# Kernel optimization log

Hardware: AMD Instinct MI355X
Metric: run time of the kernel (lower is better)

Reference implementation:

```python
import jax, jax.numpy as jnp
import numpy as np
import math

D_MODEL = 1024
NUM_HEADS = 16
SEQ = 2048
BATCH = 2


def setup_inputs() -> dict:
    key = jax.random.key(0)
    ks = jax.random.split(key, 12)
    s = 1.0 / math.sqrt(D_MODEL)
    inp = {
        "query": jax.random.normal(ks[0], (SEQ, BATCH, D_MODEL), jnp.float32),
        "key": jax.random.normal(ks[1], (SEQ, BATCH, D_MODEL), jnp.float32),
        "value": jax.random.normal(ks[2], (SEQ, BATCH, D_MODEL), jnp.float32),
        "Wq": jax.random.normal(ks[3], (D_MODEL, D_MODEL), jnp.float32) * s,
        "bq": jax.random.normal(ks[4], (D_MODEL,), jnp.float32) * 0.01,
        "Wk": jax.random.normal(ks[5], (D_MODEL, D_MODEL), jnp.float32) * s,
        "bk": jax.random.normal(ks[6], (D_MODEL,), jnp.float32) * 0.01,
        "Wv": jax.random.normal(ks[7], (D_MODEL, D_MODEL), jnp.float32) * s,
        "bv": jax.random.normal(ks[8], (D_MODEL,), jnp.float32) * 0.01,
        "Wo": jax.random.normal(ks[9], (D_MODEL, D_MODEL), jnp.float32) * s,
        "bo": jax.random.normal(ks[10], (D_MODEL,), jnp.float32) * 0.01,
    }
    # causal (subsequent) mask: True above the diagonal means masked
    inp["attn_mask"] = jnp.triu(jnp.ones((SEQ, SEQ), bool), k=1)
    # key_padding_mask: True = padding; random lengths in [SEQ//2, SEQ]
    lengths = jax.random.randint(ks[11], (BATCH,), SEQ // 2, SEQ + 1)
    inp["key_padding_mask"] = jnp.arange(SEQ)[None, :] >= lengths[:, None]
    return inp


def reference(query, key, value, Wq, bq, Wk, bk, Wv, bv, Wo, bo, attn_mask, key_padding_mask):
    S, B, D = query.shape
    H = NUM_HEADS
    dk = D // H

    def proj_split(x, W, b):
        y = x @ W.T + b                      # [S, B, D]
        return y.reshape(S, B, H, dk).transpose(1, 2, 0, 3)  # [B, H, S, dk]

    q = proj_split(query, Wq, bq)
    k = proj_split(key, Wk, bk)
    v = proj_split(value, Wv, bv)

    scores = jnp.einsum("bhqd,bhkd->bhqk", q, k) / jnp.sqrt(jnp.float32(dk))
    mask = key_padding_mask[:, None, None, :] | attn_mask[None, None, :, :]
    scores = jnp.where(mask, -jnp.inf, scores)
    p = jax.nn.softmax(scores, axis=-1)       # [B, H, S, S]
    x = jnp.einsum("bhqk,bhkd->bhqd", p, v)   # [B, H, S, dk]
    x = x.transpose(2, 0, 1, 3).reshape(S, B, D)
    return x @ Wo.T + bo
```

## Files before the change

kernel.cpp:

```cpp
#include <hip/hip_runtime.h>
#include <hip/hip_bf16.h>

#define S_LEN 2048
#define BATCH 2
#define DMODEL 1024
#define NHEAD 16
#define DK 64

typedef __bf16 bf16_t;
typedef bf16_t bf16x4 __attribute__((ext_vector_type(4)));
typedef bf16_t bf16x8 __attribute__((ext_vector_type(8)));
typedef float floatx4 __attribute__((ext_vector_type(4)));

#define SEG  ((size_t)S_LEN * BATCH * DMODEL)
#define WSEG ((size_t)DMODEL * DMODEL)
#define CVT_TOT (3 * SEG + 4 * WSEG)

#define QSCALE 0.180336879f

__global__ void prep_lens(const unsigned char* __restrict__ am,
                          const unsigned char* __restrict__ kpm,
                          int* __restrict__ lens)
{
    __shared__ int stride_s;
    __shared__ int cnt[BATCH];
    const int t = threadIdx.x;
    if (t == 0) {
        int st;
        if (am[1]) st = 1;
        else if (am[2] | am[3]) st = 2;
        else st = 4;
        stride_s = st;
    }
    if (t < BATCH) cnt[t] = 0;
    __syncthreads();
    const int st = stride_s;
    for (int idx = t; idx < BATCH * S_LEN; idx += blockDim.x) {
        int nz = 0;
        for (int c = 0; c < st; c++) nz |= kpm[idx * st + c];
        if (nz) atomicAdd(&cnt[idx / S_LEN], 1);
    }
    __syncthreads();
    if (t < BATCH) lens[t] = S_LEN - cnt[t];
}

__global__ void cvt_all(const float* __restrict__ q, const float* __restrict__ k,
                        const float* __restrict__ v, const float* __restrict__ wq,
                        const float* __restrict__ wk, const float* __restrict__ wv,
                        const float* __restrict__ wo, bf16_t* __restrict__ out)
{
    size_t i4 = ((size_t)blockIdx.x * blockDim.x + threadIdx.x) * 4;
    const size_t stride = (size_t)gridDim.x * blockDim.x * 4;
    for (; i4 < CVT_TOT; i4 += stride) {
        const float* src;
        size_t off;
        if (i4 < SEG)                    { src = q;  off = i4; }
        else if (i4 < 2 * SEG)           { src = k;  off = i4 - SEG; }
        else if (i4 < 3 * SEG)           { src = v;  off = i4 - 2 * SEG; }
        else if (i4 < 3 * SEG + WSEG)    { src = wq; off = i4 - 3 * SEG; }
        else if (i4 < 3 * SEG + 2 * WSEG){ src = wk; off = i4 - (3 * SEG + WSEG); }
        else if (i4 < 3 * SEG + 3 * WSEG){ src = wv; off = i4 - (3 * SEG + 2 * WSEG); }
        else                             { src = wo; off = i4 - (3 * SEG + 3 * WSEG); }
        const float4 x = *(const float4*)(src + off);
        bf16x4 r;
        r[0] = (bf16_t)x.x; r[1] = (bf16_t)x.y; r[2] = (bf16_t)x.z; r[3] = (bf16_t)x.w;
        *(bf16x4*)(out + i4) = r;
    }
}

__global__ __launch_bounds__(256, 2)
void gemm_qkv(const bf16_t* __restrict__ Abase, const bf16_t* __restrict__ Wbase,
              const float* __restrict__ bq, const float* __restrict__ bk,
              const float* __restrict__ bv, bf16_t* __restrict__ Obase)
{
    __shared__ bf16_t As[128 * 32];
    __shared__ bf16_t Bs[128 * 32];

    const int z = blockIdx.z;
    const bf16_t* A = Abase + (size_t)z * SEG;
    const bf16_t* W = Wbase + (size_t)z * WSEG;
    const float* bias = (z == 0) ? bq : (z == 1) ? bk : bv;
    bf16_t* C = Obase + (size_t)z * SEG;

    const int t    = threadIdx.x;
    const int wave = t >> 6;
    const int lane = t & 63;
    const int l15  = lane & 15;
    const int quad = lane >> 4;

    const int mBase = blockIdx.y * 128;
    const int nBase = blockIdx.x * 128;
    const int wRow  = (wave >> 1) * 64;
    const int wCol  = (wave & 1) * 64;

    floatx4 acc[4][4];
#pragma unroll
    for (int i = 0; i < 4; i++)
#pragma unroll
        for (int j = 0; j < 4; j++) acc[i][j] = (floatx4){0.f, 0.f, 0.f, 0.f};

    for (int k0 = 0; k0 < DMODEL; k0 += 32) {
#pragma unroll
        for (int c = 0; c < 2; c++) {
            const int chunk = c * 256 + t;
            const int row   = chunk >> 2;
            const int col   = (chunk & 3) * 8;
            const bf16_t* gA = A + (size_t)(mBase + row) * DMODEL + k0 + col;
            const bf16_t* gB = W + (size_t)(nBase + row) * DMODEL + k0 + col;
            bf16_t* lA = As + (c * 256 + wave * 64) * 8;
            bf16_t* lB = Bs + (c * 256 + wave * 64) * 8;
            __builtin_amdgcn_global_load_lds(
                (const __attribute__((address_space(1))) void*)gA,
                (__attribute__((address_space(3))) void*)lA, 16, 0, 0);
            __builtin_amdgcn_global_load_lds(
                (const __attribute__((address_space(1))) void*)gB,
                (__attribute__((address_space(3))) void*)lB, 16, 0, 0);
        }
        __syncthreads();

        bf16x8 af[4], bfr[4];
#pragma unroll
        for (int mi = 0; mi < 4; mi++)
            af[mi] = *(const bf16x8*)(As + (wRow + mi * 16 + l15) * 32 + quad * 8);
#pragma unroll
        for (int ni = 0; ni < 4; ni++)
            bfr[ni] = *(const bf16x8*)(Bs + (wCol + ni * 16 + l15) * 32 + quad * 8);
#pragma unroll
        for (int mi = 0; mi < 4; mi++)
#pragma unroll
            for (int ni = 0; ni < 4; ni++)
                acc[mi][ni] = __builtin_amdgcn_mfma_f32_16x16x32_bf16(
                    af[mi], bfr[ni], acc[mi][ni], 0, 0, 0);
        __syncthreads();
    }

    const float scale = (z == 0) ? QSCALE : 1.0f;
    float bvv[4];
#pragma unroll
    for (int ni = 0; ni < 4; ni++)
        bvv[ni] = bias[nBase + wCol + ni * 16 + l15];

#pragma unroll
    for (int mi = 0; mi < 4; mi++) {
#pragma unroll
        for (int ni = 0; ni < 4; ni++) {
            const int n = nBase + wCol + ni * 16 + l15;
            const int h = n >> 6, i = n & 63;
#pragma unroll
            for (int j = 0; j < 4; j++) {
                const int m = mBase + wRow + mi * 16 + quad * 4 + j;
                const int s = m >> 1, b = m & 1;
                const float v = (acc[mi][ni][j] + bvv[ni]) * scale;
                size_t off;
                if (z < 2)
                    off = ((size_t)(b * NHEAD + h) * S_LEN + s) * DK + i;
                else
                    off = ((size_t)(b * NHEAD + h) * DK + i) * S_LEN + s;
                C[off] = (bf16_t)v;
            }
        }
    }
}

__global__ __launch_bounds__(256, 3)
void attn(const bf16_t* __restrict__ qw, const bf16_t* __restrict__ kw,
          const bf16_t* __restrict__ vw, bf16_t* __restrict__ ow,
          const int* __restrict__ lens)
{
    __shared__ bf16_t Ks[2][64 * 64];
    __shared__ bf16_t Vs[2][64 * 64];
    __shared__ bf16_t Ps[4][16 * 70];

    const int t    = threadIdx.x;
    const int wave = t >> 6;
    const int lane = t & 63;
    const int l15  = lane & 15;
    const int quad = lane >> 4;
    const int qg   = lane & 48;
    const int rowbase = qg >> 2;

    const int n     = (int)(blockIdx.x + (blockIdx.y << 5));
    const int bh    = n & 31;
    const int qTile = 31 - (n >> 5);
    const int b     = bh >> 4;
    const int len   = lens[b];
    const int qBase = qTile * 64;

    const bf16_t* kbase = kw + (size_t)bh * S_LEN * DK;
    const bf16_t* vbase = vw + (size_t)bh * DK * S_LEN;

    const int dr = lane >> 3;
    const int cc = (lane & 7) ^ dr;

    const bf16_t* Qg = qw + ((size_t)bh * S_LEN + qBase + wave * 16) * DK;
    const bf16x8 qa0 = *(const bf16x8*)(Qg + l15 * DK + quad * 8);
    const bf16x8 qa1 = *(const bf16x8*)(Qg + l15 * DK + 32 + quad * 8);

    floatx4 O[4];
#pragma unroll
    for (int i = 0; i < 4; i++) O[i] = (floatx4){0.f, 0.f, 0.f, 0.f};
    float lrow = 0.f;

    const int ktEnd = min(qTile, (len - 1) >> 6);

    auto dma_tile = [&](int ktB, int buf) {
#pragma unroll
        for (int i = 0; i < 2; i++) {
            const int R0 = (wave * 2 + i) * 8;
            const bf16_t* gK = kbase + (size_t)(ktB + R0 + dr) * DK + cc * 8;
            const bf16_t* gV = vbase + (size_t)(R0 + dr) * S_LEN + ktB + cc * 8;
            bf16_t* lK = &Ks[buf][(size_t)R0 * 64];
            bf16_t* lV = &Vs[buf][(size_t)R0 * 64];
            __builtin_amdgcn_global_load_lds(
                (const __attribute__((address_space(1))) void*)gK,
                (__attribute__((address_space(3))) void*)lK, 16, 0, 0);
            __builtin_amdgcn_global_load_lds(
                (const __attribute__((address_space(1))) void*)gV,
                (__attribute__((address_space(3))) void*)lV, 16, 0, 0);
        }
    };

    dma_tile(0, 0);
    __syncthreads();

    const int sw  = l15 & 7;
    const int ch0 = (quad ^ sw) * 8;
    const int ch1 = ((4 | quad) ^ sw) * 8;

    for (int kt = 0; kt <= ktEnd; kt++) {
        const int cur = kt & 1;
        if (kt < ktEnd) dma_tile((kt + 1) * 64, cur ^ 1);

        floatx4 sc[4];
#pragma unroll
        for (int ni = 0; ni < 4; ni++) {
            const bf16_t* kr = &Ks[cur][(ni * 16 + l15) * 64];
            const bf16x8 kf0 = *(const bf16x8*)(kr + ch0);
            const bf16x8 kf1 = *(const bf16x8*)(kr + ch1);
            floatx4 zz = (floatx4){0.f, 0.f, 0.f, 0.f};
            zz = __builtin_amdgcn_mfma_f32_16x16x32_bf16(kf0, qa0, zz, 0, 0, 0);
            zz = __builtin_amdgcn_mfma_f32_16x16x32_bf16(kf1, qa1, zz, 0, 0, 0);
            sc[ni] = zz;
        }

        const int ktBase = kt * 64;
        const int q = qBase + wave * 16 + l15;
        const bool needMask = (kt == qTile) || (ktBase + 64 > len);
        if (needMask) {
#pragma unroll
            for (int ni = 0; ni < 4; ni++) {
#pragma unroll
                for (int r = 0; r < 4; r++) {
                    const int key = ktBase + ni * 16 + quad * 4 + r;
                    if (key > q || key >= len) sc[ni][r] = -3.0e38f;
                }
            }
        }

        float lsum = 0.f;
#pragma unroll
        for (int ni = 0; ni < 4; ni++) {
#pragma unroll
            for (int r = 0; r < 4; r++) {
                const float p = exp2f(sc[ni][r]);
                sc[ni][r] = p;
                lsum += p;
            }
        }
        lrow += lsum;

        bf16_t* Pw = Ps[wave];
#pragma unroll
        for (int ni = 0; ni < 4; ni++) {
            bf16x4 pk;
            pk[0] = (bf16_t)sc[ni][0]; pk[1] = (bf16_t)sc[ni][1];
            pk[2] = (bf16_t)sc[ni][2]; pk[3] = (bf16_t)sc[ni][3];
            *(bf16x4*)(Pw + l15 * 70 + ni * 16 + quad * 4) = pk;
        }

        const bf16x8 pa0 = *(const bf16x8*)(Pw + l15 * 70 + quad * 8);
        const bf16x8 pa1 = *(const bf16x8*)(Pw + l15 * 70 + 32 + quad * 8);
#pragma unroll
        for (int nd = 0; nd < 4; nd++) {
            const bf16_t* vr = &Vs[cur][(nd * 16 + l15) * 64];
            const bf16x8 vb0 = *(const bf16x8*)(vr + ch0);
            const bf16x8 vb1 = *(const bf16x8*)(vr + ch1);
            O[nd] = __builtin_amdgcn_mfma_f32_16x16x32_bf16(pa0, vb0, O[nd], 0, 0, 0);
            O[nd] = __builtin_amdgcn_mfma_f32_16x16x32_bf16(pa1, vb1, O[nd], 0, 0, 0);
        }
        __syncthreads();
    }

    lrow += __shfl_xor(lrow, 16);
    lrow += __shfl_xor(lrow, 32);

    float rinv[4];
#pragma unroll
    for (int j = 0; j < 4; j++)
        rinv[j] = 1.0f / __shfl(lrow, qg | (rowbase + j));
#pragma unroll
    for (int nd = 0; nd < 4; nd++) {
        const int d = (bh & 15) * DK + nd * 16 + l15;
#pragma unroll
        for (int j = 0; j < 4; j++) {
            const int qq = qBase + wave * 16 + quad * 4 + j;
            ow[((size_t)qq * BATCH + b) * DMODEL + d] = (bf16_t)(O[nd][j] * rinv[j]);
        }
    }
}

__global__ __launch_bounds__(256, 2)
void gemm_o(const bf16_t* __restrict__ A, const bf16_t* __restrict__ W,
            const float* __restrict__ bias, float* __restrict__ C)
{
    __shared__ bf16_t As[128 * 32];
    __shared__ bf16_t Bs[64 * 32];

    const int t    = threadIdx.x;
    const int wave = t >> 6;
    const int lane = t & 63;
    const int l15  = lane & 15;
    const int quad = lane >> 4;

    const int mBase = blockIdx.y * 128;
    const int nBase = blockIdx.x * 64;
    const int wRow  = wave * 32;

    floatx4 acc[2][4];
#pragma unroll
    for (int i = 0; i < 2; i++)
#pragma unroll
        for (int j = 0; j < 4; j++) acc[i][j] = (floatx4){0.f, 0.f, 0.f, 0.f};

    for (int k0 = 0; k0 < DMODEL; k0 += 32) {
#pragma unroll
        for (int c = 0; c < 2; c++) {
            const int chunk = c * 256 + t;
            const int row   = chunk >> 2;
            const int col   = (chunk & 3) * 8;
            const bf16_t* gA = A + (size_t)(mBase + row) * DMODEL + k0 + col;
            bf16_t* lA = As + (c * 256 + wave * 64) * 8;
            __builtin_amdgcn_global_load_lds(
                (const __attribute__((address_space(1))) void*)gA,
                (__attribute__((address_space(3))) void*)lA, 16, 0, 0);
        }
        {
            const int row = t >> 2;
            const int col = (t & 3) * 8;
            const bf16_t* gB = W + (size_t)(nBase + row) * DMODEL + k0 + col;
            bf16_t* lB = Bs + (wave * 64) * 8;
            __builtin_amdgcn_global_load_lds(
                (const __attribute__((address_space(1))) void*)gB,
                (__attribute__((address_space(3))) void*)lB, 16, 0, 0);
        }
        __syncthreads();

        bf16x8 af[2], bfr[4];
#pragma unroll
        for (int mi = 0; mi < 2; mi++)
            af[mi] = *(const bf16x8*)(As + (wRow + mi * 16 + l15) * 32 + quad * 8);
#pragma unroll
        for (int ni = 0; ni < 4; ni++)
            bfr[ni] = *(const bf16x8*)(Bs + (ni * 16 + l15) * 32 + quad * 8);
#pragma unroll
        for (int mi = 0; mi < 2; mi++)
#pragma unroll
            for (int ni = 0; ni < 4; ni++)
                acc[mi][ni] = __builtin_amdgcn_mfma_f32_16x16x32_bf16(
                    af[mi], bfr[ni], acc[mi][ni], 0, 0, 0);
        __syncthreads();
    }

    float bvv[4];
#pragma unroll
    for (int ni = 0; ni < 4; ni++)
        bvv[ni] = bias[nBase + ni * 16 + l15];

#pragma unroll
    for (int mi = 0; mi < 2; mi++) {
#pragma unroll
        for (int ni = 0; ni < 4; ni++) {
            const int n = nBase + ni * 16 + l15;
#pragma unroll
            for (int j = 0; j < 4; j++) {
                const int m = mBase + wRow + mi * 16 + quad * 4 + j;
                C[(size_t)m * DMODEL + n] = acc[mi][ni][j] + bvv[ni];
            }
        }
    }
}

extern "C" void kernel_launch(void* const* d_in, const int* in_sizes, int n_in,
                              void* d_out, int out_size, void* d_ws, size_t ws_size,
                              hipStream_t stream)
{
    const float* query = (const float*)d_in[0];
    const float* key   = (const float*)d_in[1];
    const float* value = (const float*)d_in[2];
    const float* Wq = (const float*)d_in[3];
    const float* bq = (const float*)d_in[4];
    const float* Wk = (const float*)d_in[5];
    const float* bk = (const float*)d_in[6];
    const float* Wv = (const float*)d_in[7];
    const float* bv = (const float*)d_in[8];
    const float* Wo = (const float*)d_in[9];
    const float* bo = (const float*)d_in[10];
    const unsigned char* am  = (const unsigned char*)d_in[11];
    const unsigned char* kpm = (const unsigned char*)d_in[12];

    bf16_t* cvt   = (bf16_t*)d_ws;
    bf16_t* q_bf  = cvt;
    bf16_t* wq_bf = cvt + 3 * SEG;
    bf16_t* wo_bf = wq_bf + 3 * WSEG;
    bf16_t* q_ws  = cvt + CVT_TOT;
    bf16_t* k_ws  = q_ws + SEG;
    bf16_t* v_ws  = k_ws + SEG;
    bf16_t* o_ws  = q_bf;
    int*    lens  = (int*)(v_ws + SEG);

    prep_lens<<<1, 256, 0, stream>>>(am, kpm, lens);
    cvt_all<<<4096, 256, 0, stream>>>(query, key, value, Wq, Wk, Wv, Wo, cvt);

    gemm_qkv<<<dim3(DMODEL / 128, (S_LEN * BATCH) / 128, 3), dim3(256), 0, stream>>>(
        q_bf, wq_bf, bq, bk, bv, q_ws);

    attn<<<dim3(32, BATCH * NHEAD), dim3(256), 0, stream>>>(
        q_ws, k_ws, v_ws, o_ws, lens);

    gemm_o<<<dim3(DMODEL / 64, (S_LEN * BATCH) / 128), dim3(256), 0, stream>>>(
        o_ws, wo_bf, bo, (float*)d_out);
}
```

Baseline: 273.3 us.

## Raise attention occupancy with a swizzled P buffer and reordered block-to-tile mapping

The padded 16x70 per-wave P staging buffer becomes an unpadded 16x64 XOR-swizzled layout. This cuts shared memory enough that the launch bound can go from 3 to 4 blocks per CU. The mapping from block index to (batch-head, query tile) also changes: groups of 8 heads interleave, and the causal tile order flips for the middle quarters, so heavy and light causal tiles mix. The reorder drops the previous heavy-first scheduling, which may hurt tail balance, and the tighter launch bound may cost registers.

```diff
diff --git a/kernel.cpp b/kernel.cpp
--- a/kernel.cpp
+++ b/kernel.cpp
@@ -162,14 +162,14 @@
     }
 }
 
-__global__ __launch_bounds__(256, 3)
+__global__ __launch_bounds__(256, 4)
 void attn(const bf16_t* __restrict__ qw, const bf16_t* __restrict__ kw,
           const bf16_t* __restrict__ vw, bf16_t* __restrict__ ow,
           const int* __restrict__ lens)
 {
     __shared__ bf16_t Ks[2][64 * 64];
     __shared__ bf16_t Vs[2][64 * 64];
-    __shared__ bf16_t Ps[4][16 * 70];
+    __shared__ bf16_t Ps[4][16 * 64];
 
     const int t    = threadIdx.x;
     const int wave = t >> 6;
@@ -179,9 +179,12 @@
     const int qg   = lane & 48;
     const int rowbase = qg >> 2;
 
-    const int n     = (int)(blockIdx.x + (blockIdx.y << 5));
-    const int bh    = n & 31;
-    const int qTile = 31 - (n >> 5);
+    const int n  = (int)(blockIdx.x + (blockIdx.y << 5));
+    const int r  = n >> 8;
+    const int j  = (n >> 3) & 31;
+    const int bh = (n & 7) | (r << 3);
+    const int flip  = (r == 1) | (r == 2);
+    const int qTile = flip ? (31 - j) : j;
     const int b     = bh >> 4;
     const int len   = lens[b];
     const int qBase = qTile * 64;
@@ -250,9 +253,9 @@
 #pragma unroll
             for (int ni = 0; ni < 4; ni++) {
 #pragma unroll
-                for (int r = 0; r < 4; r++) {
-                    const int key = ktBase + ni * 16 + quad * 4 + r;
-                    if (key > q || key >= len) sc[ni][r] = -3.0e38f;
+                for (int rr = 0; rr < 4; rr++) {
+                    const int key = ktBase + ni * 16 + quad * 4 + rr;
+                    if (key > q || key >= len) sc[ni][rr] = -3.0e38f;
                 }
             }
         }
@@ -261,9 +264,9 @@
 #pragma unroll
         for (int ni = 0; ni < 4; ni++) {
 #pragma unroll
-            for (int r = 0; r < 4; r++) {
-                const float p = exp2f(sc[ni][r]);
-                sc[ni][r] = p;
+            for (int rr = 0; rr < 4; rr++) {
+                const float p = exp2f(sc[ni][rr]);
+                sc[ni][rr] = p;
                 lsum += p;
             }
         }
@@ -275,11 +278,12 @@
             bf16x4 pk;
             pk[0] = (bf16_t)sc[ni][0]; pk[1] = (bf16_t)sc[ni][1];
             pk[2] = (bf16_t)sc[ni][2]; pk[3] = (bf16_t)sc[ni][3];
-            *(bf16x4*)(Pw + l15 * 70 + ni * 16 + quad * 4) = pk;
-        }
-
-        const bf16x8 pa0 = *(const bf16x8*)(Pw + l15 * 70 + quad * 8);
-        const bf16x8 pa1 = *(const bf16x8*)(Pw + l15 * 70 + 32 + quad * 8);
+            const int lc = 2 * ni + (quad >> 1);
+            *(bf16x4*)(Pw + l15 * 64 + ((lc ^ sw) << 3) + (quad & 1) * 4) = pk;
+        }
+
+        const bf16x8 pa0 = *(const bf16x8*)(Pw + l15 * 64 + ((quad ^ sw) << 3));
+        const bf16x8 pa1 = *(const bf16x8*)(Pw + l15 * 64 + (((4 | quad) ^ sw) << 3));
 #pragma unroll
         for (int nd = 0; nd < 4; nd++) {
             const bf16_t* vr = &Vs[cur][(nd * 16 + l15) * 64];
@@ -296,15 +300,15 @@
 
     float rinv[4];
 #pragma unroll
-    for (int j = 0; j < 4; j++)
-        rinv[j] = 1.0f / __shfl(lrow, qg | (rowbase + j));
+    for (int jj = 0; jj < 4; jj++)
+        rinv[jj] = 1.0f / __shfl(lrow, qg | (rowbase + jj));
 #pragma unroll
     for (int nd = 0; nd < 4; nd++) {
         const int d = (bh & 15) * DK + nd * 16 + l15;
 #pragma unroll
-        for (int j = 0; j < 4; j++) {
-            const int qq = qBase + wave * 16 + quad * 4 + j;
-            ow[((size_t)qq * BATCH + b) * DMODEL + d] = (bf16_t)(O[nd][j] * rinv[j]);
+        for (int jj = 0; jj < 4; jj++) {
+            const int qq = qBase + wave * 16 + quad * 4 + jj;
+            ow[((size_t)qq * BATCH + b) * DMODEL + d] = (bf16_t)(O[nd][jj] * rinv[jj]);
         }
     }
 }
```

Result: faster. 244.3 us (-10.6%).
